# Kernel tuning notes

Hardware: AMD Instinct MI355X
Metric: run time of the kernel (lower is better)

The kernel has to match this reference:

```python
import jax, jax.numpy as jnp
import numpy as np
import math

B, S, D, H = 2, 2048, 1024, 16
HD = D // H  # head dim = 64


def _rope_tables():
    # RoFormer sinusoidal position embedding: one frequency per (even, odd) pair
    pos = jnp.arange(S, dtype=jnp.float32)[:, None]                # [S, 1]
    inv_freq = 1.0 / (10000.0 ** (jnp.arange(0, HD, 2, dtype=jnp.float32) / HD))  # [HD/2]
    ang = pos * inv_freq[None, :]                                   # [S, HD/2]
    sin = jnp.sin(ang)[None, None]                                  # [1,1,S,HD/2]
    cos = jnp.cos(ang)[None, None]
    return sin, cos


def setup_inputs() -> dict:
    key = jax.random.key(0)
    k0, k1, k2, k3 = jax.random.split(key, 4)
    scale = 1.0 / math.sqrt(D)
    sin, cos = _rope_tables()
    return {
        "hidden_states": jax.random.normal(k0, (B, S, D), dtype=jnp.float32),
        "Wq": jax.random.normal(k1, (D, D), dtype=jnp.float32) * scale,
        "Wk": jax.random.normal(k2, (D, D), dtype=jnp.float32) * scale,
        "Wv": jax.random.normal(k3, (D, D), dtype=jnp.float32) * scale,
        "sin": sin,
        "cos": cos,
    }


def _split_heads(x):
    # [B,S,D] -> [B,H,S,HD]
    b, s, _ = x.shape
    return x.reshape(b, s, H, HD).transpose(0, 2, 1, 3)


def _apply_rotary(x, sin, cos):
    # x: [B,H,S,HD]; sin/cos broadcast as [1,1,S,HD/2]
    x1 = x[..., 0::2]
    x2 = x[..., 1::2]
    out = jnp.stack([x1 * cos - x2 * sin, x2 * cos + x1 * sin], axis=-1)
    return out.reshape(x.shape)


def reference(hidden_states, Wq, Wk, Wv, sin, cos):
    q = _apply_rotary(_split_heads(hidden_states @ Wq), sin, cos)  # [B,H,S,HD]
    k = _apply_rotary(_split_heads(hidden_states @ Wk), sin, cos)
    v = _apply_rotary(_split_heads(hidden_states @ Wv), sin, cos)  # note: RoPE on V too, per source
    scores = jnp.einsum("bhqd,bhkd->bhqk", q, k) / math.sqrt(HD)   # [B,H,S,S]
    probs = jax.nn.softmax(scores, axis=-1)
    ctx = jnp.einsum("bhqk,bhkd->bhqd", probs, v)                   # [B,H,S,HD]
    return ctx.transpose(0, 2, 1, 3).reshape(hidden_states.shape[0], S, D)
```

## Files before the change

kernel.cpp:

```cpp
#include <hip/hip_runtime.h>

typedef unsigned short u16;
typedef unsigned short u16x8 __attribute__((ext_vector_type(8)));
typedef unsigned short u16x4 __attribute__((ext_vector_type(4)));
typedef __bf16 bf16x8_t __attribute__((ext_vector_type(8)));
typedef float floatx4 __attribute__((ext_vector_type(4)));

#define BATCH 2
#define S_LEN 2048
#define D_DIM 1024
#define NH    16
#define HD    64

__device__ __forceinline__ u16 f2b(float f) {
  union { float f; unsigned int i; } c; c.f = f;
  const unsigned int i = c.i;
  return (u16)((i + 0x7FFFu + ((i >> 16) & 1u)) >> 16);
}
__device__ __forceinline__ bf16x8_t asbf(u16x8 v) {
  union { u16x8 u; bf16x8_t b; } c; c.u = v; return c.b;
}

__device__ __attribute__((aligned(256))) u16 g_xb[(size_t)BATCH * S_LEN * D_DIM];
__device__ __attribute__((aligned(256))) u16 g_wt[3u * D_DIM * D_DIM];
__device__ __attribute__((aligned(256))) u16 g_qkv[3u * BATCH * S_LEN * D_DIM];

__global__ __launch_bounds__(256) void convert_x(const float* __restrict__ X) {
  const size_t i = ((size_t)blockIdx.x * 256 + threadIdx.x) * 8;
  floatx4 a = *(const floatx4*)(X + i);
  floatx4 b = *(const floatx4*)(X + i + 4);
  u16x8 o;
#pragma unroll
  for (int j = 0; j < 4; ++j) { o[j] = f2b(a[j]); o[4 + j] = f2b(b[j]); }
  *(u16x8*)(g_xb + i) = o;
}

__global__ __launch_bounds__(256) void transpose_w(const float* __restrict__ W, int z) {
  __shared__ u16 t[64][65];
  u16* Wt = g_wt + (size_t)z * D_DIM * D_DIM;
  const int k0 = blockIdx.x * 64;
  const int n0 = blockIdx.y * 64;
  const int tid = threadIdx.x;
  const int rr = tid >> 4;
  const int cc = (tid & 15) * 4;
#pragma unroll
  for (int i = 0; i < 4; ++i) {
    const int r = rr + i * 16;
    floatx4 v = *(const floatx4*)(W + (size_t)(k0 + r) * D_DIM + n0 + cc);
    t[r][cc] = f2b(v[0]); t[r][cc + 1] = f2b(v[1]);
    t[r][cc + 2] = f2b(v[2]); t[r][cc + 3] = f2b(v[3]);
  }
  __syncthreads();
#pragma unroll
  for (int i = 0; i < 4; ++i) {
    const int r = rr + i * 16;
    u16x4 v;
    v[0] = t[cc][r]; v[1] = t[cc + 1][r]; v[2] = t[cc + 2][r]; v[3] = t[cc + 3][r];
    *(u16x4*)(Wt + (size_t)(n0 + r) * D_DIM + k0 + cc) = v;
  }
}

__global__ __launch_bounds__(256) void qkv_gemm(const float* __restrict__ sin_t,
                                                const float* __restrict__ cos_t) {
  __shared__ __attribute__((aligned(16))) u16 lds_a[128 * 32];
  __shared__ __attribute__((aligned(16))) u16 lds_b[128 * 32];
  const int tid = threadIdx.x;
  const int wv = tid >> 6;
  const int lane = tid & 63;
  const int lrow = lane & 15;
  const int quad = lane >> 4;
  const int wr = wv >> 1, wc = wv & 1;
  const int m0 = blockIdx.x * 128;
  const int n0 = blockIdx.y * 128;
  const int z = blockIdx.z;
  const u16* Wz = g_wt + (size_t)z * (D_DIM * D_DIM);
  u16* outz = g_qkv + (size_t)z * (BATCH * S_LEN * D_DIM);

  floatx4 acc[4][4] = {};

  const int srow = lane >> 2;
  const int scol = (lane & 3) * 8;
  const u16* gA = g_xb + (size_t)(m0 + wv * 32 + srow) * D_DIM + scol;
  const u16* gB = Wz   + (size_t)(n0 + wv * 32 + srow) * D_DIM + scol;
  u16* sA = &lds_a[(wv * 32) * 32 + lane * 8];
  u16* sB = &lds_b[(wv * 32) * 32 + lane * 8];

  for (int k0 = 0; k0 < D_DIM; k0 += 32) {
    u16x8 a0 = *(const u16x8*)(gA + k0);
    u16x8 a1 = *(const u16x8*)(gA + (size_t)16 * D_DIM + k0);
    u16x8 b0 = *(const u16x8*)(gB + k0);
    u16x8 b1 = *(const u16x8*)(gB + (size_t)16 * D_DIM + k0);
    __syncthreads();
    *(u16x8*)sA = a0; *(u16x8*)(sA + 512) = a1;
    *(u16x8*)sB = b0; *(u16x8*)(sB + 512) = b1;
    __syncthreads();
    u16x8 af[4], bfr[4];
#pragma unroll
    for (int mi = 0; mi < 4; ++mi)
      af[mi] = *(const u16x8*)&lds_a[(wr * 64 + mi * 16 + lrow) * 32 + quad * 8];
#pragma unroll
    for (int ni = 0; ni < 4; ++ni)
      bfr[ni] = *(const u16x8*)&lds_b[(wc * 64 + ni * 16 + lrow) * 32 + quad * 8];
#pragma unroll
    for (int mi = 0; mi < 4; ++mi)
#pragma unroll
      for (int ni = 0; ni < 4; ++ni)
        acc[mi][ni] = __builtin_amdgcn_mfma_f32_16x16x32_bf16(
            asbf(af[mi]), asbf(bfr[ni]), acc[mi][ni], 0, 0, 0);
  }

#pragma unroll
  for (int mi = 0; mi < 4; ++mi) {
    const int m = m0 + wr * 64 + mi * 16 + quad * 4;
    const int b = m >> 11;
#pragma unroll
    for (int ni = 0; ni < 4; ++ni) {
      const int n = n0 + wc * 64 + ni * 16 + lrow;
      const int h = n >> 6, hd = n & 63;
      const int i0 = hd >> 1;
      const float sgn = (hd & 1) ? 1.f : -1.f;
      u16* op = outz + (((size_t)(b * NH + h) * S_LEN + (m & 2047)) * HD + hd);
#pragma unroll
      for (int r = 0; r < 4; ++r) {
        const int s = (m + r) & 2047;
        const float c  = cos_t[(size_t)s * 32 + i0];
        const float sn = sin_t[(size_t)s * 32 + i0];
        const float v = acc[mi][ni][r];
        const float vp = __shfl_xor(v, 1);
        op[r * HD] = f2b(v * c + sgn * sn * vp);
      }
    }
  }
}

__global__ __launch_bounds__(256) void flash_attn(float* __restrict__ out) {
  __shared__ __attribute__((aligned(16))) u16 lds_k[64 * 72];
  __shared__ __attribute__((aligned(16))) u16 lds_v[64 * 64];
  __shared__ __attribute__((aligned(16))) u16 lds_p[4][16 * 64];
  const int bh = blockIdx.x;
  const int qt = blockIdx.y;
  const int b = bh >> 4, h = bh & 15;
  const int tid = threadIdx.x, wv = tid >> 6, lane = tid & 63;
  const int lrow = lane & 15, quad = lane >> 4;
  const u16* Qb = g_qkv + (size_t)bh * (S_LEN * HD);
  const u16* Kb = g_qkv + (size_t)(BATCH * NH + bh) * (S_LEN * HD);
  const u16* Vb = g_qkv + (size_t)(2 * BATCH * NH + bh) * (S_LEN * HD);
  const int q0 = qt * 64 + wv * 16;

  u16x8 qf[2];
#pragma unroll
  for (int ks = 0; ks < 2; ++ks)
    qf[ks] = *(const u16x8*)(Qb + (size_t)(q0 + lrow) * HD + ks * 32 + quad * 8);

  floatx4 oacc[4] = {};
  float l_part[4] = {0.f, 0.f, 0.f, 0.f};
  const float cexp = 0.125f * 1.44269504088896f;

  const int sr = tid >> 3;
  const int sc = (tid & 7) * 8;
  u16* lp = lds_p[wv];

  for (int t = 0; t < S_LEN / 64; ++t) {
    const int kv0 = t * 64;
#pragma unroll
    for (int i = 0; i < 2; ++i) {
      const int r = sr + i * 32;
      u16x8 kk = *(const u16x8*)(Kb + (size_t)(kv0 + r) * HD + sc);
      *(u16x8*)&lds_k[r * 72 + sc] = kk;
      u16x8 vvv = *(const u16x8*)(Vb + (size_t)(kv0 + r) * HD + sc);
#pragma unroll
      for (int j = 0; j < 8; ++j) {
        const int key = ((r >> 3) ^ (tid & 7) ^ j) & 7;
        lds_v[(sc + j) * 64 + key * 8 + (r & 7)] = vvv[j];
      }
    }
    __syncthreads();

    floatx4 sacc[4] = {};
#pragma unroll
    for (int nb = 0; nb < 4; ++nb)
#pragma unroll
      for (int ks = 0; ks < 2; ++ks) {
        u16x8 kf = *(const u16x8*)&lds_k[(nb * 16 + lrow) * 72 + ks * 32 + quad * 8];
        sacc[nb] = __builtin_amdgcn_mfma_f32_16x16x32_bf16(
            asbf(qf[ks]), asbf(kf), sacc[nb], 0, 0, 0);
      }

#pragma unroll
    for (int nb = 0; nb < 4; ++nb) {
      const int kvhi = 2 * nb + (lrow >> 3);
#pragma unroll
      for (int r = 0; r < 4; ++r) {
        const float p = exp2f(sacc[nb][r] * cexp);
        l_part[r] += p;
        const int q = quad * 4 + r;
        const int key = (kvhi ^ (q & 7) ^ ((q >> 3) << 1)) & 7;
        lp[q * 64 + key * 8 + (lrow & 7)] = f2b(p);
      }
    }

#pragma unroll
    for (int ks = 0; ks < 2; ++ks) {
      const int keyp = ((ks * 4 + quad) ^ (lrow & 7) ^ ((lrow >> 3) << 1)) & 7;
      u16x8 pf = *(const u16x8*)&lp[lrow * 64 + keyp * 8];
#pragma unroll
      for (int hb = 0; hb < 4; ++hb) {
        const int hd = hb * 16 + lrow;
        const int keyv = ((ks * 4 + quad) ^ (hd >> 3) ^ (hd & 7)) & 7;
        u16x8 vf = *(const u16x8*)&lds_v[hd * 64 + keyv * 8];
        oacc[hb] = __builtin_amdgcn_mfma_f32_16x16x32_bf16(
            asbf(pf), asbf(vf), oacc[hb], 0, 0, 0);
      }
    }
    __syncthreads();
  }

  float l_i[4];
#pragma unroll
  for (int r = 0; r < 4; ++r) {
    float l = l_part[r];
#pragma unroll
    for (int d = 1; d < 16; d <<= 1) l += __shfl_xor(l, d);
    l_i[r] = l;
  }

#pragma unroll
  for (int hb = 0; hb < 4; ++hb) {
    const int hd = hb * 16 + lrow;
#pragma unroll
    for (int r = 0; r < 4; ++r) {
      const int q = q0 + quad * 4 + r;
      out[((size_t)(b * S_LEN) + q) * D_DIM + h * HD + hd] = oacc[hb][r] / l_i[r];
    }
  }
}

extern "C" void kernel_launch(void* const* d_in, const int* in_sizes, int n_in,
                              void* d_out, int out_size, void* d_ws, size_t ws_size,
                              hipStream_t stream) {
  const float* X = (const float*)d_in[0];
  const float* sin_t = (const float*)d_in[4];
  const float* cos_t = (const float*)d_in[5];

  convert_x<<<2048, 256, 0, stream>>>(X);

  for (int z = 0; z < 3; ++z)
    transpose_w<<<dim3(16, 16), 256, 0, stream>>>((const float*)d_in[1 + z], z);

  qkv_gemm<<<dim3(32, 8, 3), 256, 0, stream>>>(sin_t, cos_t);

  flash_attn<<<dim3(32, 32), 256, 0, stream>>>((float*)d_out);
}
```

Measured before the change: 219.5 us.

## Write V pre-transposed from GEMM and load GEMM tiles directly into LDS

The V projection block swaps its operand roles so the accumulator comes out transposed, and it writes V as [b,h,hd,s] with RoPE applied along register pairs. The attention kernel can then copy V tiles with plain vector stores instead of a scattered per-element transpose into LDS. The GEMM main loop also switches to global_load_lds direct-to-LDS copies, which removes the register round trip. The risks are strided global writes for V^T in the GEMM epilogue and a less overlapped load pipeline.

```diff
diff --git a/kernel.cpp b/kernel.cpp
--- a/kernel.cpp
+++ b/kernel.cpp
@@ -19,6 +19,11 @@
 }
 __device__ __forceinline__ bf16x8_t asbf(u16x8 v) {
   union { u16x8 u; bf16x8_t b; } c; c.u = v; return c.b;
+}
+__device__ __forceinline__ void load_lds16(const u16* g, u16* l) {
+  __builtin_amdgcn_global_load_lds(
+      (const __attribute__((address_space(1))) void*)g,
+      (__attribute__((address_space(3))) void*)l, 16, 0, 0);
 }
 
 __device__ __attribute__((aligned(256))) u16 g_xb[(size_t)BATCH * S_LEN * D_DIM];
@@ -73,8 +78,8 @@
   const int m0 = blockIdx.x * 128;
   const int n0 = blockIdx.y * 128;
   const int z = blockIdx.z;
+  const bool vmode = (z == 2);
   const u16* Wz = g_wt + (size_t)z * (D_DIM * D_DIM);
-  u16* outz = g_qkv + (size_t)z * (BATCH * S_LEN * D_DIM);
 
   floatx4 acc[4][4] = {};
 
@@ -82,25 +87,26 @@
   const int scol = (lane & 3) * 8;
   const u16* gA = g_xb + (size_t)(m0 + wv * 32 + srow) * D_DIM + scol;
   const u16* gB = Wz   + (size_t)(n0 + wv * 32 + srow) * D_DIM + scol;
-  u16* sA = &lds_a[(wv * 32) * 32 + lane * 8];
-  u16* sB = &lds_b[(wv * 32) * 32 + lane * 8];
+  u16* sA = &lds_a[(wv * 32) * 32];
+  u16* sB = &lds_b[(wv * 32) * 32];
+
+  const u16* Aarr = vmode ? lds_b : lds_a;
+  const u16* Barr = vmode ? lds_a : lds_b;
 
   for (int k0 = 0; k0 < D_DIM; k0 += 32) {
-    u16x8 a0 = *(const u16x8*)(gA + k0);
-    u16x8 a1 = *(const u16x8*)(gA + (size_t)16 * D_DIM + k0);
-    u16x8 b0 = *(const u16x8*)(gB + k0);
-    u16x8 b1 = *(const u16x8*)(gB + (size_t)16 * D_DIM + k0);
-    __syncthreads();
-    *(u16x8*)sA = a0; *(u16x8*)(sA + 512) = a1;
-    *(u16x8*)sB = b0; *(u16x8*)(sB + 512) = b1;
+    __syncthreads();
+    load_lds16(gA + k0, sA);
+    load_lds16(gA + (size_t)16 * D_DIM + k0, sA + 512);
+    load_lds16(gB + k0, sB);
+    load_lds16(gB + (size_t)16 * D_DIM + k0, sB + 512);
     __syncthreads();
     u16x8 af[4], bfr[4];
 #pragma unroll
     for (int mi = 0; mi < 4; ++mi)
-      af[mi] = *(const u16x8*)&lds_a[(wr * 64 + mi * 16 + lrow) * 32 + quad * 8];
+      af[mi] = *(const u16x8*)&Aarr[(wr * 64 + mi * 16 + lrow) * 32 + quad * 8];
 #pragma unroll
     for (int ni = 0; ni < 4; ++ni)
-      bfr[ni] = *(const u16x8*)&lds_b[(wc * 64 + ni * 16 + lrow) * 32 + quad * 8];
+      bfr[ni] = *(const u16x8*)&Barr[(wc * 64 + ni * 16 + lrow) * 32 + quad * 8];
 #pragma unroll
     for (int mi = 0; mi < 4; ++mi)
 #pragma unroll
@@ -109,25 +115,50 @@
             asbf(af[mi]), asbf(bfr[ni]), acc[mi][ni], 0, 0, 0);
   }
 
-#pragma unroll
-  for (int mi = 0; mi < 4; ++mi) {
-    const int m = m0 + wr * 64 + mi * 16 + quad * 4;
-    const int b = m >> 11;
-#pragma unroll
-    for (int ni = 0; ni < 4; ++ni) {
-      const int n = n0 + wc * 64 + ni * 16 + lrow;
-      const int h = n >> 6, hd = n & 63;
-      const int i0 = hd >> 1;
-      const float sgn = (hd & 1) ? 1.f : -1.f;
-      u16* op = outz + (((size_t)(b * NH + h) * S_LEN + (m & 2047)) * HD + hd);
-#pragma unroll
-      for (int r = 0; r < 4; ++r) {
-        const int s = (m + r) & 2047;
-        const float c  = cos_t[(size_t)s * 32 + i0];
-        const float sn = sin_t[(size_t)s * 32 + i0];
-        const float v = acc[mi][ni][r];
-        const float vp = __shfl_xor(v, 1);
-        op[r * HD] = f2b(v * c + sgn * sn * vp);
+  if (!vmode) {
+    u16* outz = g_qkv + (size_t)z * (BATCH * S_LEN * D_DIM);
+#pragma unroll
+    for (int mi = 0; mi < 4; ++mi) {
+      const int m = m0 + wr * 64 + mi * 16 + quad * 4;
+      const int b = m >> 11;
+#pragma unroll
+      for (int ni = 0; ni < 4; ++ni) {
+        const int n = n0 + wc * 64 + ni * 16 + lrow;
+        const int h = n >> 6, hd = n & 63;
+        const int i0 = hd >> 1;
+        const float sgn = (hd & 1) ? 1.f : -1.f;
+        u16* op = outz + (((size_t)(b * NH + h) * S_LEN + (m & 2047)) * HD + hd);
+#pragma unroll
+        for (int r = 0; r < 4; ++r) {
+          const int s = (m + r) & 2047;
+          const float c  = cos_t[(size_t)s * 32 + i0];
+          const float sn = sin_t[(size_t)s * 32 + i0];
+          const float v = acc[mi][ni][r];
+          const float vp = __shfl_xor(v, 1);
+          op[r * HD] = f2b(v * c + sgn * sn * vp);
+        }
+      }
+    }
+  } else {
+    u16* outv = g_qkv + (size_t)2 * (BATCH * S_LEN * D_DIM);
+#pragma unroll
+    for (int mi = 0; mi < 4; ++mi) {
+      const int hb = n0 + wr * 64 + mi * 16 + quad * 4;
+#pragma unroll
+      for (int ni = 0; ni < 4; ++ni) {
+        const int sg = m0 + wc * 64 + ni * 16 + lrow;
+        const int b = sg >> 11, s = sg & 2047;
+#pragma unroll
+        for (int r = 0; r < 4; ++r) {
+          const int hdg = hb + r;
+          const int h = (hdg >> 6) & 15, hd = hdg & 63;
+          const float c  = cos_t[(size_t)s * 32 + (hd >> 1)];
+          const float sn = sin_t[(size_t)s * 32 + (hd >> 1)];
+          const float v  = acc[mi][ni][r];
+          const float vp = acc[mi][ni][r ^ 1];
+          const float val = (r & 1) ? (v * c + sn * vp) : (v * c - sn * vp);
+          outv[((size_t)(b * NH + h) * HD + hd) * S_LEN + s] = f2b(val);
+        }
       }
     }
   }
@@ -135,16 +166,16 @@
 
 __global__ __launch_bounds__(256) void flash_attn(float* __restrict__ out) {
   __shared__ __attribute__((aligned(16))) u16 lds_k[64 * 72];
-  __shared__ __attribute__((aligned(16))) u16 lds_v[64 * 64];
+  __shared__ __attribute__((aligned(16))) u16 lds_v[64 * 72];
   __shared__ __attribute__((aligned(16))) u16 lds_p[4][16 * 64];
   const int bh = blockIdx.x;
   const int qt = blockIdx.y;
   const int b = bh >> 4, h = bh & 15;
   const int tid = threadIdx.x, wv = tid >> 6, lane = tid & 63;
   const int lrow = lane & 15, quad = lane >> 4;
-  const u16* Qb = g_qkv + (size_t)bh * (S_LEN * HD);
-  const u16* Kb = g_qkv + (size_t)(BATCH * NH + bh) * (S_LEN * HD);
-  const u16* Vb = g_qkv + (size_t)(2 * BATCH * NH + bh) * (S_LEN * HD);
+  const u16* Qb  = g_qkv + (size_t)bh * (S_LEN * HD);
+  const u16* Kb  = g_qkv + (size_t)(BATCH * NH + bh) * (S_LEN * HD);
+  const u16* VTb = g_qkv + (size_t)(2 * BATCH * NH + bh) * (S_LEN * HD);
   const int q0 = qt * 64 + wv * 16;
 
   u16x8 qf[2];
@@ -165,14 +196,10 @@
 #pragma unroll
     for (int i = 0; i < 2; ++i) {
       const int r = sr + i * 32;
-      u16x8 kk = *(const u16x8*)(Kb + (size_t)(kv0 + r) * HD + sc);
-      *(u16x8*)&lds_k[r * 72 + sc] = kk;
-      u16x8 vvv = *(const u16x8*)(Vb + (size_t)(kv0 + r) * HD + sc);
-#pragma unroll
-      for (int j = 0; j < 8; ++j) {
-        const int key = ((r >> 3) ^ (tid & 7) ^ j) & 7;
-        lds_v[(sc + j) * 64 + key * 8 + (r & 7)] = vvv[j];
-      }
+      *(u16x8*)&lds_k[r * 72 + sc] =
+          *(const u16x8*)(Kb + (size_t)(kv0 + r) * HD + sc);
+      *(u16x8*)&lds_v[r * 72 + sc] =
+          *(const u16x8*)(VTb + (size_t)r * S_LEN + kv0 + sc);
     }
     __syncthreads();
 
@@ -205,9 +232,7 @@
       u16x8 pf = *(const u16x8*)&lp[lrow * 64 + keyp * 8];
 #pragma unroll
       for (int hb = 0; hb < 4; ++hb) {
-        const int hd = hb * 16 + lrow;
-        const int keyv = ((ks * 4 + quad) ^ (hd >> 3) ^ (hd & 7)) & 7;
-        u16x8 vf = *(const u16x8*)&lds_v[hd * 64 + keyv * 8];
+        u16x8 vf = *(const u16x8*)&lds_v[(hb * 16 + lrow) * 72 + ks * 32 + quad * 8];
         oacc[hb] = __builtin_amdgcn_mfma_f32_16x16x32_bf16(
             asbf(pf), asbf(vf), oacc[hb], 0, 0, 0);
       }
```

Result: no change. 222.4 us (+1.3%).
